# Kernel optimization log

Hardware: AMD Instinct MI355X
Metric: run time of the kernel (lower is better)

The kernel has to match this reference:

```python
import jax, jax.numpy as jnp
import numpy as np


def setup_inputs() -> dict:
    key = jax.random.key(0)
    k1, k2, k3, k4 = jax.random.split(key, 4)
    B, V, P, C, R, N, OUT = 8, 4096, 32, 32, 2, 16, 32  # N=(l_max+1)^2, l_max=3
    signal = jax.random.normal(k1, (B, V, C), dtype=jnp.float32)
    patches_idx = jax.random.randint(k2, (B, V, P), 0, V, dtype=jnp.int32)
    conv_kernel = jax.random.normal(k3, (B, V, P, R, N), dtype=jnp.float32)
    kernel_weights = jax.random.normal(k4, (OUT, C, R, N), dtype=jnp.float32) * 0.05
    biases = jnp.zeros((OUT,), dtype=jnp.float32)
    return {
        "signal": signal,
        "patches_idx": patches_idx,
        "conv_kernel": conv_kernel,
        "kernel_weights": kernel_weights,
        "biases": biases,
    }


def reference(signal, patches_idx, conv_kernel, kernel_weights, biases):
    # Gather per-vertex tree-neighbor patches (tf.gather_nd with batch idx):
    # signal [B,V,C], patches_idx [B,V,P] -> patches [B,V,P,C]
    patches = jax.vmap(lambda s, i: s[i])(signal, patches_idx)
    # Bilinear contraction with precomputed SH conv kernel: [B,V,P,R,N] x [B,V,P,C]
    y = jnp.einsum('bvprn,bvpc->bvcrn', conv_kernel, patches)
    # Learned weights contraction: [OUT,C,R,N] x [B,V,C,R,N] -> [B,V,OUT]
    y = jnp.einsum('ijrn,bvjrn->bvi', kernel_weights, y)
    y = y + biases
    return jax.nn.relu(y)
```

## Files before the change

### kernel.cpp

```cpp
#include <hip/hip_runtime.h>


typedef __attribute__((ext_vector_type(8))) short bf16x8;
typedef __attribute__((ext_vector_type(16))) float f32x16;
typedef __attribute__((ext_vector_type(4))) float f32x4;

__device__ __forceinline__ unsigned short f2bf(float f) {
    union { float f; unsigned int u; } x;
    x.f = f;
    unsigned int u = x.u;
    return (unsigned short)((u + 0x7fffu + ((u >> 16) & 1u)) >> 16);
}

__global__ __launch_bounds__(256) void prep_w_kernel(
        const float* __restrict__ W, unsigned short* __restrict__ Wf) {
    int tid = blockIdx.x * 256 + threadIdx.x;
    int j = tid & 7;
    int l = (tid >> 3) & 63;
    int pair = tid >> 9;
    int s = pair >> 1;
    int t = pair & 1;
    int i = 16 * t + (l & 15);
    int crn = 32 * s + 8 * (l >> 4) + j;
    Wf[tid] = f2bf(W[i * 1024 + crn]);
}

__global__ __launch_bounds__(256) void fused_kernel(
        const float* __restrict__ sig, const int* __restrict__ pidx,
        const float* __restrict__ ck, const unsigned short* __restrict__ Wf,
        const float* __restrict__ bias, float* __restrict__ out) {
    __shared__ __align__(16) unsigned short T_lds[16 * 1032];
    const int tid = threadIdx.x;
    const int l = tid & 63;
    const int w = tid >> 6;
    const int m0 = blockIdx.x * 16;
    const int b = m0 >> 12;
    const int cc = l & 31;
    const int g = l >> 5;
    const float* sgb = sig + (size_t)b * (4096 * 32);

    for (int q = 0; q < 4; ++q) {
        const int bvl = w * 4 + q;
        const int m = m0 + bvl;
        const int* idxp = pidx + (size_t)m * 32;
        const float* kt = ck + (size_t)m * 1024;
        f32x16 acc = {};
        #pragma unroll
        for (int half = 0; half < 2; ++half) {
            bf16x8 af, bfr;
            #pragma unroll
            for (int j = 0; j < 8; ++j) {
                const int p = half * 16 + 8 * g + j;
                const int row = idxp[p];
                af[j]  = (short)f2bf(sgb[row * 32 + cc]);
                bfr[j] = (short)f2bf(kt[p * 32 + cc]);
            }
            acc = __builtin_amdgcn_mfma_f32_32x32x16_bf16(af, bfr, acc, 0, 0, 0);
        }
        unsigned short* trow = T_lds + bvl * 1032;
        #pragma unroll
        for (int r = 0; r < 16; ++r) {
            const int ct = (r & 3) + 8 * (r >> 2) + 4 * g;
            trow[ct * 32 + cc] = f2bf(acc[r]);
        }
    }
    __syncthreads();

    f32x4 acc0 = {}, acc1 = {};
    const int lg = l >> 4;
    const int ln = l & 15;
    #pragma unroll
    for (int si = 0; si < 8; ++si) {
        const int s = 8 * w + si;
        const bf16x8 af = *(const bf16x8*)(T_lds + ln * 1032 + s * 32 + 8 * lg);
        const bf16x8* wrow = (const bf16x8*)(Wf + (size_t)(s * 2) * 512);
        const bf16x8 b0 = wrow[l];
        const bf16x8 b1 = wrow[64 + l];
        acc0 = __builtin_amdgcn_mfma_f32_16x16x32_bf16(af, b0, acc0, 0, 0, 0);
        acc1 = __builtin_amdgcn_mfma_f32_16x16x32_bf16(af, b1, acc1, 0, 0, 0);
    }
    __syncthreads();

    float* red = (float*)T_lds;
    {
        f32x4* rp = (f32x4*)(red + w * 512);
        rp[l]      = acc0;
        rp[64 + l] = acc1;
    }
    __syncthreads();

    #pragma unroll
    for (int o0 = 0; o0 < 2; ++o0) {
        const int o = o0 * 256 + tid;
        float sum = red[o] + red[512 + o] + red[1024 + o] + red[1536 + o];
        const int t  = o >> 8;
        const int ll = (o >> 2) & 63;
        const int r  = o & 3;
        const int bv = ((ll >> 4) << 2) + r;
        const int i  = 16 * t + (ll & 15);
        sum += bias[i];
        out[(size_t)(m0 + bv) * 32 + i] = sum > 0.f ? sum : 0.f;
    }
}

extern "C" void kernel_launch(void* const* d_in, const int* in_sizes, int n_in,
                              void* d_out, int out_size, void* d_ws, size_t ws_size,
                              hipStream_t stream) {
    const float* sig  = (const float*)d_in[0];
    const int*   pidx = (const int*)d_in[1];
    const float* ck   = (const float*)d_in[2];
    const float* W    = (const float*)d_in[3];
    const float* bias = (const float*)d_in[4];
    float* out = (float*)d_out;
    unsigned short* Wf = (unsigned short*)d_ws;

    prep_w_kernel<<<128, 256, 0, stream>>>(W, Wf);
    fused_kernel<<<2048, 256, 0, stream>>>(sig, pidx, ck, Wf, bias, out);
}
```

Measured before the change: 40.83 us.

## Drop weight prep kernel, truncate conv kernel via high-half loads, simplify rounding

Removes the separate weight conversion kernel launch and instead has each block load fp32 weights directly and convert them to bf16 in registers. The conv kernel is read as only the upper 16 bits of each float, so the conversion becomes truncation and only half the bytes are requested, though each 2-byte load is strided over 4-byte elements. The rounding helper switches from round-to-nearest-even to a cheaper round-half-up. Per-block weight loads and conversions are now repeated across all blocks, and the truncation slightly changes numerics.

```diff
diff --git a/kernel.cpp b/kernel.cpp
--- a/kernel.cpp
+++ b/kernel.cpp
@@ -5,29 +5,15 @@
 typedef __attribute__((ext_vector_type(16))) float f32x16;
 typedef __attribute__((ext_vector_type(4))) float f32x4;
 
-__device__ __forceinline__ unsigned short f2bf(float f) {
+__device__ __forceinline__ unsigned short f2bf_rh(float f) {
     union { float f; unsigned int u; } x;
     x.f = f;
-    unsigned int u = x.u;
-    return (unsigned short)((u + 0x7fffu + ((u >> 16) & 1u)) >> 16);
-}
-
-__global__ __launch_bounds__(256) void prep_w_kernel(
-        const float* __restrict__ W, unsigned short* __restrict__ Wf) {
-    int tid = blockIdx.x * 256 + threadIdx.x;
-    int j = tid & 7;
-    int l = (tid >> 3) & 63;
-    int pair = tid >> 9;
-    int s = pair >> 1;
-    int t = pair & 1;
-    int i = 16 * t + (l & 15);
-    int crn = 32 * s + 8 * (l >> 4) + j;
-    Wf[tid] = f2bf(W[i * 1024 + crn]);
+    return (unsigned short)((x.u + 0x8000u) >> 16);
 }
 
 __global__ __launch_bounds__(256) void fused_kernel(
         const float* __restrict__ sig, const int* __restrict__ pidx,
-        const float* __restrict__ ck, const unsigned short* __restrict__ Wf,
+        const float* __restrict__ ck, const float* __restrict__ W,
         const float* __restrict__ bias, float* __restrict__ out) {
     __shared__ __align__(16) unsigned short T_lds[16 * 1032];
     const int tid = threadIdx.x;
@@ -38,12 +24,13 @@
     const int cc = l & 31;
     const int g = l >> 5;
     const float* sgb = sig + (size_t)b * (4096 * 32);
+    const unsigned short* ckh = (const unsigned short*)ck;
 
     for (int q = 0; q < 4; ++q) {
         const int bvl = w * 4 + q;
         const int m = m0 + bvl;
         const int* idxp = pidx + (size_t)m * 32;
-        const float* kt = ck + (size_t)m * 1024;
+        const size_t kbase = (size_t)m * 1024;
         f32x16 acc = {};
         #pragma unroll
         for (int half = 0; half < 2; ++half) {
@@ -52,16 +39,16 @@
             for (int j = 0; j < 8; ++j) {
                 const int p = half * 16 + 8 * g + j;
                 const int row = idxp[p];
-                af[j]  = (short)f2bf(sgb[row * 32 + cc]);
-                bfr[j] = (short)f2bf(kt[p * 32 + cc]);
+                af[j]  = (short)f2bf_rh(sgb[row * 32 + cc]);
+                bfr[j] = (short)ckh[((kbase + p * 32 + cc) << 1) | 1];
             }
             acc = __builtin_amdgcn_mfma_f32_32x32x16_bf16(af, bfr, acc, 0, 0, 0);
         }
-        unsigned short* trow = T_lds + bvl * 1032;
+        unsigned short* trow = T_lds + bvl * 1032 + cc + g * 128;
         #pragma unroll
         for (int r = 0; r < 16; ++r) {
-            const int ct = (r & 3) + 8 * (r >> 2) + 4 * g;
-            trow[ct * 32 + cc] = f2bf(acc[r]);
+            const int ct = (r & 3) + 8 * (r >> 2);
+            trow[ct * 32] = f2bf_rh(acc[r]);
         }
     }
     __syncthreads();
@@ -69,13 +56,24 @@
     f32x4 acc0 = {}, acc1 = {};
     const int lg = l >> 4;
     const int ln = l & 15;
+    const float* wl0 = W + ln * 1024 + 8 * lg;
+    const float* wl1 = wl0 + 16 * 1024;
     #pragma unroll
     for (int si = 0; si < 8; ++si) {
         const int s = 8 * w + si;
         const bf16x8 af = *(const bf16x8*)(T_lds + ln * 1032 + s * 32 + 8 * lg);
-        const bf16x8* wrow = (const bf16x8*)(Wf + (size_t)(s * 2) * 512);
-        const bf16x8 b0 = wrow[l];
-        const bf16x8 b1 = wrow[64 + l];
+        f32x4 wa0 = *(const f32x4*)(wl0 + 32 * s);
+        f32x4 wa1 = *(const f32x4*)(wl0 + 32 * s + 4);
+        f32x4 wb0 = *(const f32x4*)(wl1 + 32 * s);
+        f32x4 wb1 = *(const f32x4*)(wl1 + 32 * s + 4);
+        bf16x8 b0, b1;
+        #pragma unroll
+        for (int j = 0; j < 4; ++j) {
+            b0[j]     = (short)f2bf_rh(wa0[j]);
+            b0[4 + j] = (short)f2bf_rh(wa1[j]);
+            b1[j]     = (short)f2bf_rh(wb0[j]);
+            b1[4 + j] = (short)f2bf_rh(wb1[j]);
+        }
         acc0 = __builtin_amdgcn_mfma_f32_16x16x32_bf16(af, b0, acc0, 0, 0, 0);
         acc1 = __builtin_amdgcn_mfma_f32_16x16x32_bf16(af, b1, acc1, 0, 0, 0);
     }
@@ -112,8 +110,6 @@
     const float* W    = (const float*)d_in[3];
     const float* bias = (const float*)d_in[4];
     float* out = (float*)d_out;
-    unsigned short* Wf = (unsigned short*)d_ws;
 
-    prep_w_kernel<<<128, 256, 0, stream>>>(W, Wf);
-    fused_kernel<<<2048, 256, 0, stream>>>(sig, pidx, ck, Wf, bias, out);
+    fused_kernel<<<2048, 256, 0, stream>>>(sig, pidx, ck, W, bias, out);
 }
```

Result: slower. 59.05 us (+44.6%).
